# Performance work log

Measured on AMD Instinct MI355X. Metric: run time of the kernel, lower is better.

Reference implementation:

```python
import jax, jax.numpy as jnp
import numpy as np

B, E, H = 131072, 128, 128


def setup_inputs() -> dict:
    key = jax.random.key(0)
    ks = jax.random.split(key, 14)
    s_in = 1.0 / np.sqrt(E)
    s_h = 1.0 / np.sqrt(H)
    return {
        "x": jax.random.normal(ks[0], (B, E), jnp.float32),
        "hidden_memory_tm1": jax.random.normal(ks[1], (2, B, H), jnp.float32),
        "Wi": jax.random.normal(ks[2], (E, H), jnp.float32) * s_in,
        "Ui": jax.random.normal(ks[3], (H, H), jnp.float32) * s_h,
        "bi": jax.random.normal(ks[4], (H,), jnp.float32) * 0.1,
        "Wf": jax.random.normal(ks[5], (E, H), jnp.float32) * s_in,
        "Uf": jax.random.normal(ks[6], (H, H), jnp.float32) * s_h,
        "bf": jax.random.normal(ks[7], (H,), jnp.float32) * 0.1,
        "Wog": jax.random.normal(ks[8], (E, H), jnp.float32) * s_in,
        "Uog": jax.random.normal(ks[9], (H, H), jnp.float32) * s_h,
        "bog": jax.random.normal(ks[10], (H,), jnp.float32) * 0.1,
        "Wc": jax.random.normal(ks[11], (E, H), jnp.float32) * s_in,
        "Uc": jax.random.normal(ks[12], (H, H), jnp.float32) * s_h,
        "bc": jax.random.normal(ks[13], (H,), jnp.float32) * 0.1,
    }


def reference(x, hidden_memory_tm1, Wi, Ui, bi, Wf, Uf, bf, Wog, Uog, bog, Wc, Uc, bc):
    h_prev, c_prev = hidden_memory_tm1[0], hidden_memory_tm1[1]
    # Fuse the 8 small matmuls into 2 concatenated GEMMs (same math, gate order i,f,o,c)
    W = jnp.concatenate([Wi, Wf, Wog, Wc], axis=1)   # [E, 4H]
    U = jnp.concatenate([Ui, Uf, Uog, Uc], axis=1)   # [H, 4H]
    b = jnp.concatenate([bi, bf, bog, bc], axis=0)   # [4H]
    gates = x @ W + h_prev @ U + b                   # [B, 4H]
    gi, gf, go, gc = jnp.split(gates, 4, axis=1)
    i = jax.nn.sigmoid(gi)
    f = jax.nn.sigmoid(gf)
    o = jax.nn.sigmoid(go)
    c_ = jnp.tanh(gc)
    c = f * c_prev + i * c_
    h = o * jnp.tanh(c)
    return jnp.stack([h, c])  # [2, B, H]
```

## Files before the change

### kernel.cpp

```cpp
#include <hip/hip_runtime.h>
#include <hip/hip_bf16.h>
#include <stdint.h>


#define NB 131072
#define KDIM 256
#define NDIM 512
#define BM 64

typedef __attribute__((ext_vector_type(4))) float f32x4;
typedef __attribute__((ext_vector_type(8))) short s16x8;

__device__ __forceinline__ unsigned short f2bf(float f) {
    union { float f; unsigned int u; } v; v.f = f;
    unsigned int u = v.u;
    unsigned int r = u + 0x7FFFu + ((u >> 16) & 1u);
    return (unsigned short)(r >> 16);
}
__device__ __forceinline__ float bf2f(unsigned short h) {
    union { float f; unsigned int u; } v; v.u = ((unsigned int)h) << 16;
    return v.f;
}
__device__ __forceinline__ float sigmoid_f(float x) {
    return 1.0f / (1.0f + __expf(-x));
}
__device__ __forceinline__ float tanh_f(float x) {
    float e = __expf(2.0f * x);
    return 1.0f - 2.0f / (e + 1.0f);
}

__global__ void pack_weights(const float* __restrict__ Wi, const float* __restrict__ Ui,
                             const float* __restrict__ Wf, const float* __restrict__ Uf,
                             const float* __restrict__ Wo, const float* __restrict__ Uo,
                             const float* __restrict__ Wc, const float* __restrict__ Uc,
                             unsigned short* __restrict__ Bhi, unsigned short* __restrict__ Blo) {
    int tid = blockIdx.x * blockDim.x + threadIdx.x;
    if (tid >= 8 * 32 * 64) return;
    int lane = tid & 63;
    int jg   = (tid >> 6) & 31;
    int kf   = tid >> 11;

    int j  = jg * 16 + (lane & 15);
    int g  = j >> 7;
    int jj = j & 127;
    const float* W = (g == 0) ? Wi : (g == 1) ? Wf : (g == 2) ? Wo : Wc;
    const float* U = (g == 0) ? Ui : (g == 1) ? Uf : (g == 2) ? Uo : Uc;

    int k0 = kf * 32 + ((lane >> 4) << 3);
    s16x8 h8, l8;
    #pragma unroll
    for (int e = 0; e < 8; ++e) {
        int k = k0 + e;
        float v = (k < 128) ? W[k * 128 + jj] : U[(k - 128) * 128 + jj];
        unsigned short h = f2bf(v);
        float r = v - bf2f(h);
        h8[e] = (short)h;
        l8[e] = (short)f2bf(r);
    }
    size_t off = (size_t)tid * 8;
    *reinterpret_cast<s16x8*>(Bhi + off) = h8;
    *reinterpret_cast<s16x8*>(Blo + off) = l8;
}

__global__ __launch_bounds__(512, 2) void lstm_main(
        const float* __restrict__ x, const float* __restrict__ hprev,
        const float* __restrict__ cprev,
        const unsigned short* __restrict__ Bhi, const unsigned short* __restrict__ Blo,
        const float* __restrict__ bi, const float* __restrict__ bf_,
        const float* __restrict__ bo, const float* __restrict__ bc,
        float* __restrict__ hout, float* __restrict__ cout) {

    extern __shared__ unsigned short smem[];
    unsigned short* a_hi = smem;
    unsigned short* a_lo = smem + BM * KDIM;
    char* a_hi_c = reinterpret_cast<char*>(a_hi);
    char* a_lo_c = reinterpret_cast<char*>(a_lo);

    const int t    = threadIdx.x;
    const int lane = t & 63;
    const int w    = t >> 6;
    const int row0 = blockIdx.x * BM;

    #pragma unroll
    for (int s = 0; s < 8; ++s) {
        int f4  = s * 512 + t;
        int row = f4 >> 6;
        int k0  = (f4 & 63) * 4;
        const float* src = (k0 < 128)
            ? (x     + (size_t)(row0 + row) * 128 + k0)
            : (hprev + (size_t)(row0 + row) * 128 + (k0 - 128));
        f32x4 v = *reinterpret_cast<const f32x4*>(src);

        unsigned short h0 = f2bf(v.x), h1 = f2bf(v.y), h2 = f2bf(v.z), h3 = f2bf(v.w);
        unsigned short l0 = f2bf(v.x - bf2f(h0));
        unsigned short l1 = f2bf(v.y - bf2f(h1));
        unsigned short l2 = f2bf(v.z - bf2f(h2));
        unsigned short l3 = f2bf(v.w - bf2f(h3));

        uint2 hh, ll;
        hh.x = (unsigned)h0 | ((unsigned)h1 << 16);
        hh.y = (unsigned)h2 | ((unsigned)h3 << 16);
        ll.x = (unsigned)l0 | ((unsigned)l1 << 16);
        ll.y = (unsigned)l2 | ((unsigned)l3 << 16);

        int byte = (row * 512 + k0 * 2) ^ ((row & 7) << 4);
        *reinterpret_cast<uint2*>(a_hi_c + byte) = hh;
        *reinterpret_cast<uint2*>(a_lo_c + byte) = ll;
    }
    __syncthreads();

    f32x4 acc[4][4];
    #pragma unroll
    for (int m = 0; m < 4; ++m)
        #pragma unroll
        for (int g = 0; g < 4; ++g)
            acc[m][g] = (f32x4){0.f, 0.f, 0.f, 0.f};

    #pragma unroll
    for (int kf = 0; kf < 8; ++kf) {
        s16x8 af[4], al[4];
        #pragma unroll
        for (int m = 0; m < 4; ++m) {
            int row   = m * 16 + (lane & 15);
            int kbyte = kf * 64 + ((lane >> 4) << 4);
            int byte  = (row * 512 + kbyte) ^ ((row & 7) << 4);
            af[m] = *reinterpret_cast<const s16x8*>(a_hi_c + byte);
            al[m] = *reinterpret_cast<const s16x8*>(a_lo_c + byte);
        }
        #pragma unroll
        for (int g = 0; g < 4; ++g) {
            size_t boff = ((size_t)((kf * 32 + g * 8 + w) * 64 + lane)) * 8;
            s16x8 bh = *reinterpret_cast<const s16x8*>(Bhi + boff);
            s16x8 bl = *reinterpret_cast<const s16x8*>(Blo + boff);
            #pragma unroll
            for (int m = 0; m < 4; ++m) {
                acc[m][g] = __builtin_amdgcn_mfma_f32_16x16x32_bf16(af[m], bh, acc[m][g], 0, 0, 0);
                acc[m][g] = __builtin_amdgcn_mfma_f32_16x16x32_bf16(af[m], bl, acc[m][g], 0, 0, 0);
                acc[m][g] = __builtin_amdgcn_mfma_f32_16x16x32_bf16(al[m], bh, acc[m][g], 0, 0, 0);
            }
        }
    }

    const int j = w * 16 + (lane & 15);
    const float vbi = bi[j], vbf = bf_[j], vbo = bo[j], vbc = bc[j];

    #pragma unroll
    for (int m = 0; m < 4; ++m) {
        int rbase = row0 + m * 16 + ((lane >> 4) << 2);
        #pragma unroll
        for (int r = 0; r < 4; ++r) {
            size_t off = (size_t)(rbase + r) * 128 + j;
            float gi = acc[m][0][r] + vbi;
            float gf = acc[m][1][r] + vbf;
            float go = acc[m][2][r] + vbo;
            float gc = acc[m][3][r] + vbc;
            float iv = sigmoid_f(gi);
            float fv = sigmoid_f(gf);
            float ov = sigmoid_f(go);
            float cc = tanh_f(gc);
            float cp = cprev[off];
            float cn = fv * cp + iv * cc;
            float hn = ov * tanh_f(cn);
            hout[off] = hn;
            cout[off] = cn;
        }
    }
}

extern "C" void kernel_launch(void* const* d_in, const int* in_sizes, int n_in,
                              void* d_out, int out_size, void* d_ws, size_t ws_size,
                              hipStream_t stream) {
    const float* x  = (const float*)d_in[0];
    const float* hm = (const float*)d_in[1];
    const float* Wi = (const float*)d_in[2];
    const float* Ui = (const float*)d_in[3];
    const float* bi = (const float*)d_in[4];
    const float* Wf = (const float*)d_in[5];
    const float* Uf = (const float*)d_in[6];
    const float* bf = (const float*)d_in[7];
    const float* Wo = (const float*)d_in[8];
    const float* Uo = (const float*)d_in[9];
    const float* bo = (const float*)d_in[10];
    const float* Wc = (const float*)d_in[11];
    const float* Uc = (const float*)d_in[12];
    const float* bc = (const float*)d_in[13];

    const size_t BH = (size_t)NB * 128;
    const float* hprev = hm;
    const float* cprev = hm + BH;
    float* hout = (float*)d_out;
    float* cout = (float*)d_out + BH;

    unsigned short* Bhi = (unsigned short*)d_ws;
    unsigned short* Blo = Bhi + (size_t)KDIM * NDIM;

    pack_weights<<<64, 256, 0, stream>>>(Wi, Ui, Wf, Uf, Wo, Uo, Wc, Uc, Bhi, Blo);

    const int grid = NB / BM;
    lstm_main<<<grid, 512, 2 * BM * KDIM * sizeof(unsigned short), stream>>>(
        x, hprev, cprev, Bhi, Blo, bi, bf, bo, bc, hout, cout);
}
```

Before: 373.0 us.

## Make LSTM kernel persistent with double-buffered A tiles and prefetched loads

The grid becomes 256 persistent blocks, each walking 8 row tiles. Each block double-buffers the split-bf16 A operand in shared memory and holds the next tile's global loads in registers, so conversion and loading overlap with the MFMA work. It also prefetches B fragments one k-step ahead, loads cprev early, uses nontemporal loads and stores, and uses rcp intrinsics in the activations. Shared memory doubles to 128KB per block and register pressure rises, which may limit occupancy to one block per CU.

```diff
diff --git a/kernel.cpp b/kernel.cpp
--- a/kernel.cpp
+++ b/kernel.cpp
@@ -1,5 +1,4 @@
 #include <hip/hip_runtime.h>
-#include <hip/hip_bf16.h>
 #include <stdint.h>
 
 
@@ -7,26 +6,40 @@
 #define KDIM 256
 #define NDIM 512
 #define BM 64
+#define TILES 8
+#define GRID 256
 
 typedef __attribute__((ext_vector_type(4))) float f32x4;
 typedef __attribute__((ext_vector_type(8))) short s16x8;
 
-__device__ __forceinline__ unsigned short f2bf(float f) {
-    union { float f; unsigned int u; } v; v.f = f;
-    unsigned int u = v.u;
-    unsigned int r = u + 0x7FFFu + ((u >> 16) & 1u);
-    return (unsigned short)(r >> 16);
-}
-__device__ __forceinline__ float bf2f(unsigned short h) {
-    union { float f; unsigned int u; } v; v.u = ((unsigned int)h) << 16;
-    return v.f;
-}
-__device__ __forceinline__ float sigmoid_f(float x) {
-    return 1.0f / (1.0f + __expf(-x));
-}
-__device__ __forceinline__ float tanh_f(float x) {
-    float e = __expf(2.0f * x);
-    return 1.0f - 2.0f / (e + 1.0f);
+__device__ __forceinline__ float asf(unsigned u){ union{unsigned u;float f;}v; v.u=u; return v.f; }
+__device__ __forceinline__ unsigned asu(float f){ union{float f;unsigned u;}v; v.f=f; return v.u; }
+
+__device__ __forceinline__ unsigned rne(float f){
+    unsigned u = asu(f);
+    return u + 0x7FFFu + ((u >> 16) & 1u);
+}
+__device__ __forceinline__ unsigned short f2bf(float f){ return (unsigned short)(rne(f) >> 16); }
+__device__ __forceinline__ float bf2f(unsigned short h){ return asf(((unsigned)h) << 16); }
+
+__device__ __forceinline__ void cvt4(f32x4 v, uint2 &hh, uint2 &ll){
+    unsigned r0 = rne(v.x), r1 = rne(v.y), r2 = rne(v.z), r3 = rne(v.w);
+    hh.x = (r0 >> 16) | (r1 & 0xFFFF0000u);
+    hh.y = (r2 >> 16) | (r3 & 0xFFFF0000u);
+    float l0 = v.x - asf(r0 & 0xFFFF0000u);
+    float l1 = v.y - asf(r1 & 0xFFFF0000u);
+    float l2 = v.z - asf(r2 & 0xFFFF0000u);
+    float l3 = v.w - asf(r3 & 0xFFFF0000u);
+    unsigned s0 = rne(l0), s1 = rne(l1), s2 = rne(l2), s3 = rne(l3);
+    ll.x = (s0 >> 16) | (s1 & 0xFFFF0000u);
+    ll.y = (s2 >> 16) | (s3 & 0xFFFF0000u);
+}
+
+__device__ __forceinline__ float sig_f(float g){
+    return __builtin_amdgcn_rcpf(1.0f + __expf(-g));
+}
+__device__ __forceinline__ float tanh_f(float g){
+    return 1.0f - 2.0f * __builtin_amdgcn_rcpf(__expf(2.0f * g) + 1.0f);
 }
 
 __global__ void pack_weights(const float* __restrict__ Wi, const float* __restrict__ Ui,
@@ -70,101 +83,144 @@
         const float* __restrict__ bo, const float* __restrict__ bc,
         float* __restrict__ hout, float* __restrict__ cout) {
 
-    extern __shared__ unsigned short smem[];
-    unsigned short* a_hi = smem;
-    unsigned short* a_lo = smem + BM * KDIM;
-    char* a_hi_c = reinterpret_cast<char*>(a_hi);
-    char* a_lo_c = reinterpret_cast<char*>(a_lo);
+    __shared__ unsigned short smem[2][2][BM * KDIM];
 
     const int t    = threadIdx.x;
     const int lane = t & 63;
     const int w    = t >> 6;
-    const int row0 = blockIdx.x * BM;
-
-    #pragma unroll
-    for (int s = 0; s < 8; ++s) {
-        int f4  = s * 512 + t;
-        int row = f4 >> 6;
-        int k0  = (f4 & 63) * 4;
-        const float* src = (k0 < 128)
-            ? (x     + (size_t)(row0 + row) * 128 + k0)
-            : (hprev + (size_t)(row0 + row) * 128 + (k0 - 128));
-        f32x4 v = *reinterpret_cast<const f32x4*>(src);
-
-        unsigned short h0 = f2bf(v.x), h1 = f2bf(v.y), h2 = f2bf(v.z), h3 = f2bf(v.w);
-        unsigned short l0 = f2bf(v.x - bf2f(h0));
-        unsigned short l1 = f2bf(v.y - bf2f(h1));
-        unsigned short l2 = f2bf(v.z - bf2f(h2));
-        unsigned short l3 = f2bf(v.w - bf2f(h3));
-
-        uint2 hh, ll;
-        hh.x = (unsigned)h0 | ((unsigned)h1 << 16);
-        hh.y = (unsigned)h2 | ((unsigned)h3 << 16);
-        ll.x = (unsigned)l0 | ((unsigned)l1 << 16);
-        ll.y = (unsigned)l2 | ((unsigned)l3 << 16);
-
-        int byte = (row * 512 + k0 * 2) ^ ((row & 7) << 4);
-        *reinterpret_cast<uint2*>(a_hi_c + byte) = hh;
-        *reinterpret_cast<uint2*>(a_lo_c + byte) = ll;
-    }
-    __syncthreads();
-
-    f32x4 acc[4][4];
-    #pragma unroll
-    for (int m = 0; m < 4; ++m)
-        #pragma unroll
-        for (int g = 0; g < 4; ++g)
-            acc[m][g] = (f32x4){0.f, 0.f, 0.f, 0.f};
-
-    #pragma unroll
-    for (int kf = 0; kf < 8; ++kf) {
-        s16x8 af[4], al[4];
-        #pragma unroll
-        for (int m = 0; m < 4; ++m) {
-            int row   = m * 16 + (lane & 15);
-            int kbyte = kf * 64 + ((lane >> 4) << 4);
-            int byte  = (row * 512 + kbyte) ^ ((row & 7) << 4);
-            af[m] = *reinterpret_cast<const s16x8*>(a_hi_c + byte);
-            al[m] = *reinterpret_cast<const s16x8*>(a_lo_c + byte);
-        }
-        #pragma unroll
-        for (int g = 0; g < 4; ++g) {
-            size_t boff = ((size_t)((kf * 32 + g * 8 + w) * 64 + lane)) * 8;
-            s16x8 bh = *reinterpret_cast<const s16x8*>(Bhi + boff);
-            s16x8 bl = *reinterpret_cast<const s16x8*>(Blo + boff);
-            #pragma unroll
-            for (int m = 0; m < 4; ++m) {
-                acc[m][g] = __builtin_amdgcn_mfma_f32_16x16x32_bf16(af[m], bh, acc[m][g], 0, 0, 0);
-                acc[m][g] = __builtin_amdgcn_mfma_f32_16x16x32_bf16(af[m], bl, acc[m][g], 0, 0, 0);
-                acc[m][g] = __builtin_amdgcn_mfma_f32_16x16x32_bf16(al[m], bh, acc[m][g], 0, 0, 0);
-            }
-        }
-    }
 
     const int j = w * 16 + (lane & 15);
     const float vbi = bi[j], vbf = bf_[j], vbo = bo[j], vbc = bc[j];
 
-    #pragma unroll
-    for (int m = 0; m < 4; ++m) {
-        int rbase = row0 + m * 16 + ((lane >> 4) << 2);
-        #pragma unroll
-        for (int r = 0; r < 4; ++r) {
-            size_t off = (size_t)(rbase + r) * 128 + j;
-            float gi = acc[m][0][r] + vbi;
-            float gf = acc[m][1][r] + vbf;
-            float go = acc[m][2][r] + vbo;
-            float gc = acc[m][3][r] + vbc;
-            float iv = sigmoid_f(gi);
-            float fv = sigmoid_f(gf);
-            float ov = sigmoid_f(go);
-            float cc = tanh_f(gc);
-            float cp = cprev[off];
-            float cn = fv * cp + iv * cc;
-            float hn = ov * tanh_f(cn);
-            hout[off] = hn;
-            cout[off] = cn;
-        }
+    f32x4 sreg[8];
+
+    #define LOAD_A(tile_)                                                         \
+        {   const int row0_ = (tile_) * BM;                                       \
+            _Pragma("unroll")                                                     \
+            for (int s = 0; s < 8; ++s) {                                         \
+                int f4 = s * 512 + t;                                             \
+                int row = f4 >> 6, k0 = (f4 & 63) * 4;                            \
+                const float* src = (k0 < 128)                                     \
+                    ? (x     + (size_t)(row0_ + row) * 128 + k0)                  \
+                    : (hprev + (size_t)(row0_ + row) * 128 + (k0 - 128));         \
+                sreg[s] = __builtin_nontemporal_load(                             \
+                              reinterpret_cast<const f32x4*>(src));               \
+            }                                                                     \
+        }
+
+    #define CONVERT_A(buf_)                                                       \
+        {   char* hi_c = reinterpret_cast<char*>(&smem[(buf_)][0][0]);            \
+            char* lo_c = reinterpret_cast<char*>(&smem[(buf_)][1][0]);            \
+            _Pragma("unroll")                                                     \
+            for (int s = 0; s < 8; ++s) {                                         \
+                int f4 = s * 512 + t;                                             \
+                int row = f4 >> 6, k0 = (f4 & 63) * 4;                            \
+                uint2 hh, ll;                                                     \
+                cvt4(sreg[s], hh, ll);                                            \
+                int byte = (row * 512 + k0 * 2) ^ ((row & 7) << 4);               \
+                *reinterpret_cast<uint2*>(hi_c + byte) = hh;                      \
+                *reinterpret_cast<uint2*>(lo_c + byte) = ll;                      \
+            }                                                                     \
+        }
+
+    const int tile0 = blockIdx.x * TILES;
+
+    LOAD_A(tile0);
+    CONVERT_A(0);
+    LOAD_A(tile0 + 1);
+    __syncthreads();
+
+    for (int it = 0; it < TILES; ++it) {
+        const int cur = it & 1;
+
+        if (it + 1 < TILES) CONVERT_A(cur ^ 1);
+        if (it + 2 < TILES) LOAD_A(tile0 + it + 2);
+
+        const int tile = tile0 + it;
+        const int row0 = tile * BM;
+
+        float cp[4][4];
+        #pragma unroll
+        for (int m = 0; m < 4; ++m)
+            #pragma unroll
+            for (int r = 0; r < 4; ++r)
+                cp[m][r] = __builtin_nontemporal_load(
+                    cprev + (size_t)(row0 + m * 16 + ((lane >> 4) << 2) + r) * 128 + j);
+
+        f32x4 acc[4][4];
+        #pragma unroll
+        for (int m = 0; m < 4; ++m)
+            #pragma unroll
+            for (int g = 0; g < 4; ++g)
+                acc[m][g] = (f32x4){0.f, 0.f, 0.f, 0.f};
+
+        const char* hi_c = reinterpret_cast<const char*>(&smem[cur][0][0]);
+        const char* lo_c = reinterpret_cast<const char*>(&smem[cur][1][0]);
+
+        #define BOFF(kf_, g_) ((size_t)((((kf_) * 32 + (g_) * 8 + w) * 64 + lane)) * 8)
+
+        s16x8 bh[2][4], bl[2][4];
+        #pragma unroll
+        for (int g = 0; g < 4; ++g) {
+            bh[0][g] = *reinterpret_cast<const s16x8*>(Bhi + BOFF(0, g));
+            bl[0][g] = *reinterpret_cast<const s16x8*>(Blo + BOFF(0, g));
+        }
+
+        #pragma unroll
+        for (int kf = 0; kf < 8; ++kf) {
+            const int c = kf & 1, n = c ^ 1;
+            if (kf < 7) {
+                #pragma unroll
+                for (int g = 0; g < 4; ++g) {
+                    bh[n][g] = *reinterpret_cast<const s16x8*>(Bhi + BOFF(kf + 1, g));
+                    bl[n][g] = *reinterpret_cast<const s16x8*>(Blo + BOFF(kf + 1, g));
+                }
+            }
+            #pragma unroll
+            for (int m = 0; m < 4; ++m) {
+                int row   = m * 16 + (lane & 15);
+                int kbyte = kf * 64 + ((lane >> 4) << 4);
+                int byte  = (row * 512 + kbyte) ^ ((row & 7) << 4);
+                s16x8 af = *reinterpret_cast<const s16x8*>(hi_c + byte);
+                s16x8 al = *reinterpret_cast<const s16x8*>(lo_c + byte);
+                #pragma unroll
+                for (int g = 0; g < 4; ++g)
+                    acc[m][g] = __builtin_amdgcn_mfma_f32_16x16x32_bf16(af, bh[c][g], acc[m][g], 0, 0, 0);
+                #pragma unroll
+                for (int g = 0; g < 4; ++g)
+                    acc[m][g] = __builtin_amdgcn_mfma_f32_16x16x32_bf16(af, bl[c][g], acc[m][g], 0, 0, 0);
+                #pragma unroll
+                for (int g = 0; g < 4; ++g)
+                    acc[m][g] = __builtin_amdgcn_mfma_f32_16x16x32_bf16(al, bh[c][g], acc[m][g], 0, 0, 0);
+            }
+        }
+
+        #pragma unroll
+        for (int m = 0; m < 4; ++m) {
+            int rbase = row0 + m * 16 + ((lane >> 4) << 2);
+            #pragma unroll
+            for (int r = 0; r < 4; ++r) {
+                size_t off = (size_t)(rbase + r) * 128 + j;
+                float gi = acc[m][0][r] + vbi;
+                float gf = acc[m][1][r] + vbf;
+                float go = acc[m][2][r] + vbo;
+                float gc = acc[m][3][r] + vbc;
+                float iv = sig_f(gi);
+                float fv = sig_f(gf);
+                float ov = sig_f(go);
+                float cc = tanh_f(gc);
+                float cn = fv * cp[m][r] + iv * cc;
+                float hn = ov * tanh_f(cn);
+                __builtin_nontemporal_store(hn, hout + off);
+                __builtin_nontemporal_store(cn, cout + off);
+            }
+        }
+
+        __syncthreads();
     }
+    #undef LOAD_A
+    #undef CONVERT_A
+    #undef BOFF
 }
 
 extern "C" void kernel_launch(void* const* d_in, const int* in_sizes, int n_in,
@@ -196,7 +252,6 @@
 
     pack_weights<<<64, 256, 0, stream>>>(Wi, Ui, Wf, Uf, Wo, Uo, Wc, Uc, Bhi, Blo);
 
-    const int grid = NB / BM;
-    lstm_main<<<grid, 512, 2 * BM * KDIM * sizeof(unsigned short), stream>>>(
+    lstm_main<<<GRID, 512, 0, stream>>>(
         x, hprev, cprev, Bhi, Blo, bi, bf, bo, bc, hout, cout);
 }
```

Result: slower. 545.4 us (+46.2%).
